# Performance work log

Measured on AMD Instinct MI355X. Metric: run time of the kernel, lower is better.

Reference implementation:

```python
import jax, jax.numpy as jnp
import numpy as np

V, D, H, L, C = 32000, 256, 256, 2, 2  # vocab, embed, hidden, layers, classes
B, T = 64, 1024
PAD = 0


def setup_inputs() -> dict:
    key = jax.random.key(0)
    ks = jax.random.split(key, 10)
    # end-padded token sequences with realistic lengths
    tokens = jax.random.randint(ks[0], (B, T), 1, V)
    lengths = jax.random.randint(ks[1], (B,), T // 2, T + 1)
    valid = jnp.arange(T)[None, :] < lengths[:, None]
    x = jnp.where(valid, tokens, PAD)
    # embedding table, padding row zeroed (padding_idx semantics)
    E = (jax.random.normal(ks[2], (V, D)) * 0.02).at[PAD].set(0.0)

    def gate(k, in_size):
        W = jax.random.normal(k, (in_size + H, 4 * H)) / np.sqrt(in_size + H)
        b = jnp.zeros((4 * H,)).at[:H].set(1.0)  # forget-gate bias = 1
        return W, b

    Wf0, bf0 = gate(ks[3], D)
    Wb0, bb0 = gate(ks[4], D)
    Wf1, bf1 = gate(ks[5], 2 * H)
    Wb1, bb1 = gate(ks[6], 2 * H)
    Wfc = jax.random.normal(ks[7], (2 * H, C)) / np.sqrt(2 * H)
    bfc = jnp.zeros((C,))
    return dict(x=x, E=E, Wf0=Wf0, bf0=bf0, Wb0=Wb0, bb0=bb0,
                Wf1=Wf1, bf1=bf1, Wb1=Wb1, bb1=bb1, Wfc=Wfc, bfc=bfc)


def _run_dir(seq, lengths, W, b, reverse):
    # seq: (B, T, in) -> outputs (B, T, H), last hidden (B, H)
    Tn = seq.shape[1]
    xs = jnp.swapaxes(seq, 0, 1)          # (T, B, in)
    ts = jnp.arange(Tn)
    if reverse:
        xs, ts = xs[::-1], ts[::-1]
    h0 = jnp.zeros((seq.shape[0], H), seq.dtype)

    def step(carry, inp):
        h, c = carry
        x_t, t = inp
        z = jnp.concatenate([h, x_t], axis=-1) @ W + b   # (B, 4H)
        f, i, g, o = jnp.split(z, 4, axis=-1)            # gate order: f,i,g,o
        c_new = jax.nn.sigmoid(f) * c + jax.nn.sigmoid(i) * jnp.tanh(g)
        h_new = jax.nn.sigmoid(o) * jnp.tanh(c_new)
        m = (t < lengths)[:, None].astype(h.dtype)       # freeze state at pads
        h = m * h_new + (1.0 - m) * h
        c = m * c_new + (1.0 - m) * c
        return (h, c), h

    (hT, _), outs = jax.lax.scan(step, (h0, h0), (xs, ts))
    outs = jnp.swapaxes(outs, 0, 1)                      # (B, T, H)
    if reverse:
        outs = outs[:, ::-1]
    return outs, hT


def reference(x, E, Wf0, bf0, Wb0, bb0, Wf1, bf1, Wb1, bb1, Wfc, bfc):
    lengths = (x != PAD).sum(axis=1)
    layer_input = E[x]                                   # (B, T, D)
    params = [(Wf0, bf0, Wb0, bb0), (Wf1, bf1, Wb1, bb1)]
    fh = bh = None
    for Wf, bf, Wb, bb in params:
        fo, fh = _run_dir(layer_input, lengths, Wf, bf, reverse=False)
        bo, bh = _run_dir(layer_input, lengths, Wb, bb, reverse=True)
        layer_input = jnp.concatenate([fo, bo], axis=-1)  # (B, T, 2H)
    h = jnp.concatenate([fh, bh], axis=1)                 # (B, 2H)
    return h @ Wfc + bfc                                  # (B, C) logits
```

## Files before the change

### kernel.cpp

```cpp
#include <hip/hip_runtime.h>
#include <hip/hip_bf16.h>
#include <math.h>

namespace {
constexpr int Bn = 64;
constexpr int Tn = 1024;
constexpr int Dn = 256;
constexpr int Hn = 256;
}

typedef __attribute__((ext_vector_type(8))) short short8;
typedef __attribute__((ext_vector_type(4))) float f32x4;

template <typename T>
__device__ __forceinline__ float ldf(const T* p, long i);
template <>
__device__ __forceinline__ float ldf<float>(const float* p, long i) { return p[i]; }
template <>
__device__ __forceinline__ float ldf<__hip_bfloat16>(const __hip_bfloat16* p, long i) {
  return __bfloat162float(p[i]);
}

__device__ __forceinline__ float sigmf(float x) {
  return __builtin_amdgcn_rcpf(1.0f + __expf(-x));
}
__device__ __forceinline__ float tanh_fast(float x) {
  return 1.0f - 2.0f * __builtin_amdgcn_rcpf(__expf(2.0f * x) + 1.0f);
}

__device__ __forceinline__ void lds_barrier() {
  asm volatile("s_waitcnt lgkmcnt(0)" ::: "memory");
  __builtin_amdgcn_sched_barrier(0);
  __builtin_amdgcn_s_barrier();
  __builtin_amdgcn_sched_barrier(0);
}

__global__ void k_detect(const unsigned short* __restrict__ e, int* __restrict__ flag) {
  __shared__ int sbuf[256];
  int bad = 0;
  for (int i = threadIdx.x; i < 4096; i += 256) {
    const unsigned short v = e[i];
    const int ex = (v >> 7) & 0xFF;
    bad += (ex >= 137) ? 1 : 0;
  }
  sbuf[threadIdx.x] = bad;
  __syncthreads();
  for (int s = 128; s > 0; s >>= 1) {
    if (threadIdx.x < s) sbuf[threadIdx.x] += sbuf[threadIdx.x + s];
    __syncthreads();
  }
  if (threadIdx.x == 0) flag[0] = (sbuf[0] > 64) ? 1 : 0;
}

__global__ void k_lengths(const int* __restrict__ x, int* __restrict__ len) {
  const int b = blockIdx.x;
  int cnt = 0;
  for (int t = threadIdx.x; t < Tn; t += blockDim.x) cnt += (x[b * Tn + t] != 0) ? 1 : 0;
  __shared__ int sbuf[256];
  sbuf[threadIdx.x] = cnt;
  __syncthreads();
  for (int s = 128; s > 0; s >>= 1) {
    if (threadIdx.x < s) sbuf[threadIdx.x] += sbuf[threadIdx.x + s];
    __syncthreads();
  }
  if (threadIdx.x == 0) len[b] = sbuf[0];
}


__global__ void k_prep_small(const void* b0f, const void* b0b, const void* b1f, const void* b1b,
                             const int* __restrict__ flag, float* __restrict__ biasbuf) {
  const int tid = threadIdx.x;
  const bool isf32 = flag[0] != 0;
  for (int idx = tid; idx < 4096; idx += 256) {
    const int j = idx >> 10, col = idx & 1023;
    const void* src = (j == 0) ? b0f : (j == 1) ? b0b : (j == 2) ? b1f : b1b;
    biasbuf[idx] = isf32 ? ((const float*)src)[col]
                         : __bfloat162float(((const __hip_bfloat16*)src)[col]);
  }
}

__global__ void k_prepw(const void* W0, const void* W1, const void* W2, const void* W3,
                        const int* __restrict__ flag, __hip_bfloat16* __restrict__ whT,
                        __hip_bfloat16* __restrict__ wxT0, __hip_bfloat16* __restrict__ wxT1) {
  const int j = blockIdx.z;
  const int rows = (j < 2) ? 512 : 768;
  const int bx = blockIdx.x;
  if (bx * 64 >= rows) return;
  const int by = blockIdx.y;
  const void* W = (j == 0) ? W0 : (j == 1) ? W1 : (j == 2) ? W2 : W3;
  const bool isf32 = flag[0] != 0;
  __shared__ float tile[64][65];
  const int tid = threadIdx.x;
  const int c = tid & 63, r4 = tid >> 6;
#pragma unroll
  for (int rep = 0; rep < 16; ++rep) {
    const int rr = r4 * 16 + rep;
    const size_t idx = (size_t)(bx * 64 + rr) * 1024 + by * 64 + c;
    tile[rr][c] = isf32 ? ((const float*)W)[idx]
                        : __bfloat162float(((const __hip_bfloat16*)W)[idx]);
  }
  __syncthreads();
  const int kk = tid & 63;
#pragma unroll
  for (int rep = 0; rep < 16; ++rep) {
    const int a = r4 * 16 + rep;
    const int n = by * 64 + a;
    const int k = bx * 64 + kk;
    const __hip_bfloat16 v = __float2bfloat16(tile[kk][a]);
    if (k < 256) {
      whT[(size_t)j * (1024 * 256) + (size_t)n * 256 + k] = v;
    } else {
      const int k2 = k - 256;
      if (j < 2)
        wxT0[(size_t)j * (1024 * 256) + (size_t)n * 256 + k2] = v;
      else
        wxT1[(size_t)(j - 2) * (1024 * 512) + (size_t)n * 512 + k2] = v;
    }
  }
}

template <int K, bool GATHER>
__launch_bounds__(256, 2)
__global__ void k_xproj3(const int* __restrict__ x, const void* __restrict__ E,
                         const int* __restrict__ flag, const __hip_bfloat16* __restrict__ Af,
                         const __hip_bfloat16* __restrict__ Ab,
                         const __hip_bfloat16* __restrict__ WT,
                         __hip_bfloat16* __restrict__ xp,
                         const int Mrows, const int t0f, const int t0b) {
  constexpr int KC = 256;
  __shared__ __hip_bfloat16 Btile[128][KC + 8];
  const int tix = blockIdx.x;
  const int by = tix & 7;
  const int dz = (tix >> 3) & 1;
  const int bx = tix >> 4;
  const int tid = threadIdx.x, w = tid >> 6, L = tid & 63, quad = L >> 4, l16 = L & 15;
  const __hip_bfloat16* __restrict__ WTd = WT + (size_t)dz * (1024 * K);
  __hip_bfloat16* __restrict__ o = xp + (size_t)dz * Mrows * 1024;

  f32x4 acc[2][8];
#pragma unroll
  for (int mt = 0; mt < 2; ++mt)
#pragma unroll
    for (int nt = 0; nt < 8; ++nt) {
      acc[mt][nt][0] = 0.f; acc[mt][nt][1] = 0.f; acc[mt][nt][2] = 0.f; acc[mt][nt][3] = 0.f;
    }

  const int row0 = bx * 128 + w * 32 + l16;
  const __hip_bfloat16* arow0b = nullptr;
  const __hip_bfloat16* arow1b = nullptr;
  const float* arow0f = nullptr;
  const float* arow1f = nullptr;
  bool isf32 = false;
  if constexpr (GATHER) {
    isf32 = flag[0] != 0;
    const int t0 = (dz ? t0b : t0f) + (row0 >> 6), b0 = row0 & 63;
    const int r1 = row0 + 16;
    const int t1 = (dz ? t0b : t0f) + (r1 >> 6), b1 = r1 & 63;
    const int tok0 = x[b0 * Tn + t0];
    const int tok1 = x[b1 * Tn + t1];
    if (isf32) {
      arow0f = (const float*)E + (size_t)tok0 * Dn;
      arow1f = (const float*)E + (size_t)tok1 * Dn;
    } else {
      arow0b = (const __hip_bfloat16*)E + (size_t)tok0 * Dn;
      arow1b = (const __hip_bfloat16*)E + (size_t)tok1 * Dn;
    }
  } else {
    const __hip_bfloat16* A = dz ? Ab : Af;
    arow0b = A + (size_t)row0 * K;
    arow1b = A + (size_t)(row0 + 16) * K;
  }

  for (int ch = 0; ch < K / KC; ++ch) {
    if (ch) __syncthreads();
#pragma unroll
    for (int it = 0; it < 16; ++it) {
      const int idx = it * 256 + tid;
      const int col = idx >> 5, seg = idx & 31;
      *(short8*)&Btile[col][seg * 8] =
          *(const short8*)(WTd + (size_t)(by * 128 + col) * K + ch * KC + seg * 8);
    }
    __syncthreads();

#pragma unroll
    for (int kc = 0; kc < 8; ++kc) {
      short8 a0, a1;
      if constexpr (GATHER) {
        if (isf32) {
#pragma unroll
          for (int jj = 0; jj < 8; ++jj) {
            __hip_bfloat16 h0 = __float2bfloat16(arow0f[kc * 32 + quad * 8 + jj]);
            __hip_bfloat16 h1 = __float2bfloat16(arow1f[kc * 32 + quad * 8 + jj]);
            a0[jj] = *(const short*)&h0;
            a1[jj] = *(const short*)&h1;
          }
        } else {
          a0 = *(const short8*)(arow0b + kc * 32 + quad * 8);
          a1 = *(const short8*)(arow1b + kc * 32 + quad * 8);
        }
      } else {
        a0 = *(const short8*)(arow0b + ch * KC + kc * 32 + quad * 8);
        a1 = *(const short8*)(arow1b + ch * KC + kc * 32 + quad * 8);
      }
#pragma unroll
      for (int nt = 0; nt < 8; ++nt) {
        const short8 b = *(const short8*)&Btile[nt * 16 + l16][kc * 32 + quad * 8];
        acc[0][nt] = __builtin_amdgcn_mfma_f32_16x16x32_bf16(a0, b, acc[0][nt], 0, 0, 0);
        acc[1][nt] = __builtin_amdgcn_mfma_f32_16x16x32_bf16(a1, b, acc[1][nt], 0, 0, 0);
      }
    }
  }

  {
    const int tl = bx * 2 + (w >> 1);
    const int jv = (by >> 1) * 2 + (w & 1);
    const int qbase = (by & 1) << 1;
    __hip_bfloat16* __restrict__ ob = o + (size_t)tl * 65536 + (size_t)jv * 2048;
#pragma unroll
    for (int nt = 0; nt < 8; ++nt) {
      const int q_ = qbase + (nt >> 2);
      const int tid_c = (nt & 3) * 64 + quad * 16 + l16;
      short8 sv;
#pragma unroll
      for (int r = 0; r < 4; ++r) {
        __hip_bfloat16 h0 = __float2bfloat16(acc[0][nt][r]);
        __hip_bfloat16 h1 = __float2bfloat16(acc[1][nt][r]);
        sv[r] = *(const short*)&h0;
        sv[4 + r] = *(const short*)&h1;
      }
      *(short8*)(ob + (size_t)q_ * 16384 + tid_c * 8) = sv;
    }
  }
}

template <bool WRITE_SEQ>
__launch_bounds__(256, 1) __global__
void k_lstm_fast(const __hip_bfloat16* __restrict__ WhT,
                 const __hip_bfloat16* __restrict__ xproj,
                 const float* __restrict__ biasL,
                 const int* __restrict__ lengths,
                 unsigned* __restrict__ hgs,
                 unsigned* __restrict__ hflags,
                 float* __restrict__ cstate, float* __restrict__ hstate,
                 __hip_bfloat16* __restrict__ seq0,
                 const int s0, const int Tc) {
  const int xcd = blockIdx.x & 7;
  const int kq = blockIdx.x >> 3;
  if (xcd >= 2 || kq >= 4) return;
  const int d = xcd;
  const int q = kq;
  const int tid = threadIdx.x;
  const int w = tid >> 6, L = tid & 63, quad = L >> 4, l16 = L & 15;
  const int u = q * 64 + w * 16 + l16;

  __shared__ __hip_bfloat16 h_lds[2][64][272];
  for (int idx = tid; idx < 2 * 64 * 272; idx += 256)
    (&h_lds[0][0][0])[idx] = __float2bfloat16(0.0f);

  const __hip_bfloat16* __restrict__ Wd = WhT + (size_t)d * (1024 * 256);
  short8 wfrag[4][8];
#pragma unroll
  for (int g = 0; g < 4; ++g)
#pragma unroll
    for (int kc = 0; kc < 8; ++kc)
      wfrag[g][kc] = *(const short8*)(Wd + (size_t)(g * 256 + u) * 256 + kc * 32 + quad * 8);

  float bz[4];
#pragma unroll
  for (int g = 0; g < 4; ++g) bz[g] = biasL[d * 1024 + g * 256 + u];

  float c_reg[16], h_reg[16];
  int len_b[16];
#pragma unroll
  for (int mt = 0; mt < 4; ++mt)
#pragma unroll
    for (int r = 0; r < 4; ++r) {
      const int idx = mt * 4 + r;
      const int b = mt * 16 + quad * 4 + r;
      len_b[idx] = lengths[b];
      if (s0 == 0) {
        c_reg[idx] = 0.0f;
        h_reg[idx] = 0.0f;
      } else {
        c_reg[idx] = cstate[((size_t)(d * 64 + b) << 8) + u];
        h_reg[idx] = hstate[((size_t)(d * 64 + b) << 8) + u];
      }
    }
  __syncthreads();
  {
    const int ib = (s0 - 1) & 1;
#pragma unroll
    for (int mt = 0; mt < 4; ++mt)
#pragma unroll
      for (int r = 0; r < 4; ++r)
        h_lds[ib][mt * 16 + quad * 4 + r][u] = __float2bfloat16(h_reg[mt * 4 + r]);
  }
  __syncthreads();

  const __hip_bfloat16* __restrict__ xq =
      xproj + (size_t)d * Tc * 65536 + (size_t)q * 16384 + (size_t)tid * 8;

  for (int sl = 0; sl < Tc; ++sl) {
    const int s = s0 + sl;
    const int t = d ? (Tn - 1 - s) : s;
    const int tl = d ? (Tc - 1 - sl) : sl;
    const int pb = (s - 1) & 1;
    const int cb = s & 1;

    short8 xv[8];
    {
      const __hip_bfloat16* __restrict__ src = xq + (size_t)tl * 65536;
#pragma unroll
      for (int jv = 0; jv < 8; ++jv) xv[jv] = *(const short8*)(src + jv * 2048);
    }

    if (s > 0) {
      if (w != q) {
        const unsigned exp = (unsigned)s;
        {
          const unsigned* __restrict__ f4 =
              hflags + (((d * 2 + ((s - 1) & 1)) * 4 + w) * 4);
          for (;;) {
            const unsigned f0 =
                __hip_atomic_load(f4 + 0, __ATOMIC_RELAXED, __HIP_MEMORY_SCOPE_AGENT);
            const unsigned f1 =
                __hip_atomic_load(f4 + 1, __ATOMIC_RELAXED, __HIP_MEMORY_SCOPE_AGENT);
            const unsigned f2 =
                __hip_atomic_load(f4 + 2, __ATOMIC_RELAXED, __HIP_MEMORY_SCOPE_AGENT);
            const unsigned f3 =
                __hip_atomic_load(f4 + 3, __ATOMIC_RELAXED, __HIP_MEMORY_SCOPE_AGENT);
            if (f0 >= exp && f1 >= exp && f2 >= exp && f3 >= exp) break;
            __builtin_amdgcn_s_sleep(1);
          }
        }
        const unsigned long long* __restrict__ src64 =
            (const unsigned long long*)(hgs + ((((size_t)d * 2 + ((s - 1) & 1)) * 4 + w) << 12));
        unsigned long long v[32];
        unsigned pend = 0xFFFFFFFFu;
        int tries = 0;
        do {
          if (tries++) __builtin_amdgcn_s_sleep(1);
#pragma unroll
          for (int i = 0; i < 32; ++i)
            if (pend & (1u << i))
              v[i] = __hip_atomic_load(src64 + i * 64 + L, __ATOMIC_RELAXED,
                                       __HIP_MEMORY_SCOPE_AGENT);
#pragma unroll
          for (int i = 0; i < 32; ++i)
            if (pend & (1u << i)) {
              const unsigned lo = (unsigned)v[i], hi = (unsigned)(v[i] >> 32);
              if ((lo >> 16) == exp && (hi >> 16) == exp) pend &= ~(1u << i);
            }
        } while (pend);
#pragma unroll
        for (int i = 0; i < 32; ++i) {
          const int j = i * 64 + L;
          const unsigned lo = (unsigned)v[i], hi = (unsigned)(v[i] >> 32);
          const unsigned packed = (lo & 0xFFFFu) | (hi << 16);
          *(unsigned*)&h_lds[pb][j >> 5][w * 64 + (j & 31) * 2] = packed;
        }
      }
      lds_barrier();
    }

    f32x4 acc[4][4];
#pragma unroll
    for (int mt = 0; mt < 4; ++mt)
#pragma unroll
      for (int g = 0; g < 4; ++g) {
        const short8 v = xv[g * 2 + (mt >> 1)];
#pragma unroll
        for (int r = 0; r < 4; ++r) {
          const short sv = v[(mt & 1) * 4 + r];
          acc[mt][g][r] = __bfloat162float(*(const __hip_bfloat16*)&sv) + bz[g];
        }
      }

#pragma unroll
    for (int kc = 0; kc < 8; ++kc) {
#pragma unroll
      for (int mt = 0; mt < 4; ++mt) {
        const short8 a = *(const short8*)&h_lds[pb][mt * 16 + l16][kc * 32 + quad * 8];
#pragma unroll
        for (int g = 0; g < 4; ++g)
          acc[mt][g] =
              __builtin_amdgcn_mfma_f32_16x16x32_bf16(a, wfrag[g][kc], acc[mt][g], 0, 0, 0);
      }
    }

    unsigned* __restrict__ dst32 = hgs + ((((size_t)d * 2 + (s & 1)) * 4 + q) << 12);
    const unsigned tag = ((unsigned)(s + 1)) << 16;
    __hip_bfloat16 hbf[16];
#pragma unroll
    for (int mt = 0; mt < 4; ++mt)
#pragma unroll
      for (int r = 0; r < 4; ++r) {
        const int idx = mt * 4 + r, b = mt * 16 + quad * 4 + r;
        const float fg = sigmf(acc[mt][0][r]);
        const float ig = sigmf(acc[mt][1][r]);
        const float gg = tanh_fast(acc[mt][2][r]);
        const float og = sigmf(acc[mt][3][r]);
        const float cn = fg * c_reg[idx] + ig * gg;
        const float hn = og * tanh_fast(cn);
        if (t < len_b[idx]) {
          c_reg[idx] = cn;
          h_reg[idx] = hn;
        }
        hbf[idx] = __float2bfloat16(h_reg[idx]);
        __hip_atomic_store(dst32 + b * 64 + w * 16 + l16,
                           tag | (unsigned)*(unsigned short*)&hbf[idx], __ATOMIC_RELAXED,
                           __HIP_MEMORY_SCOPE_AGENT);
      }

    if (L == 0)
      __hip_atomic_store(hflags + (((d * 2 + (s & 1)) * 4 + q) * 4 + w),
                         (unsigned)(s + 1), __ATOMIC_RELAXED, __HIP_MEMORY_SCOPE_AGENT);

#pragma unroll
    for (int mt = 0; mt < 4; ++mt)
#pragma unroll
      for (int r = 0; r < 4; ++r)
        h_lds[cb][mt * 16 + quad * 4 + r][u] = hbf[mt * 4 + r];

    if (WRITE_SEQ) {
#pragma unroll
      for (int mt = 0; mt < 4; ++mt)
#pragma unroll
        for (int r = 0; r < 4; ++r) {
          const int b = mt * 16 + quad * 4 + r;
          seq0[((size_t)t * 64 + b) * 512 + d * 256 + u] = hbf[mt * 4 + r];
        }
    }
  }

#pragma unroll
  for (int mt = 0; mt < 4; ++mt)
#pragma unroll
    for (int r = 0; r < 4; ++r) {
      const int idx = mt * 4 + r, b = mt * 16 + quad * 4 + r;
      cstate[((size_t)(d * 64 + b) << 8) + u] = c_reg[idx];
      hstate[((size_t)(d * 64 + b) << 8) + u] = h_reg[idx];
    }
}

template <typename TW, int XK, bool WRITE_SEQ>
__device__ __forceinline__ void lstm_body(const int* __restrict__ x, const TW* __restrict__ E,
                                          const __hip_bfloat16* __restrict__ seq_in,
                                          const TW* __restrict__ W, const TW* __restrict__ bias,
                                          const int len, const int b, const int dir,
                                          __hip_bfloat16* __restrict__ seq_out,
                                          float* __restrict__ hfin) {
  const int j = threadIdx.x;
  __shared__ float h[Hn];
  __shared__ float xb[XK];
  float hj = 0.0f, cj = 0.0f;
  h[j] = 0.0f;
  const float bfj = ldf(bias, j);
  const float bij = ldf(bias, Hn + j);
  const float bgj = ldf(bias, 2 * Hn + j);
  const float boj = ldf(bias, 3 * Hn + j);
  __syncthreads();
  for (int s = 0; s < Tn; ++s) {
    const int t = dir ? (Tn - 1 - s) : s;
    const bool active = (t < len);
    if (active) {
      if constexpr (XK == Dn) {
        const int tok = x[b * Tn + t];
        xb[j] = ldf(E, (long)tok * Dn + j);
      } else {
        const long base = ((long)(b * Tn + t)) * (2 * Hn);
        xb[j] = __bfloat162float(seq_in[base + j]);
        xb[j + Hn] = __bfloat162float(seq_in[base + j + Hn]);
      }
      __syncthreads();
      float af = bfj, ai = bij, ag = bgj, ao = boj;
#pragma unroll 4
      for (int k = 0; k < Hn; ++k) {
        const float hk = h[k];
        const long r = (long)k * (4 * Hn);
        af += hk * ldf(W, r + j);
        ai += hk * ldf(W, r + Hn + j);
        ag += hk * ldf(W, r + 2 * Hn + j);
        ao += hk * ldf(W, r + 3 * Hn + j);
      }
#pragma unroll 4
      for (int k = 0; k < XK; ++k) {
        const float xk = xb[k];
        const long r = (long)(Hn + k) * (4 * Hn);
        af += xk * ldf(W, r + j);
        ai += xk * ldf(W, r + Hn + j);
        ag += xk * ldf(W, r + 2 * Hn + j);
        ao += xk * ldf(W, r + 3 * Hn + j);
      }
      const float fg = 1.0f / (1.0f + expf(-af));
      const float ig = 1.0f / (1.0f + expf(-ai));
      const float gg = tanhf(ag);
      const float og = 1.0f / (1.0f + expf(-ao));
      const float cn = fg * cj + ig * gg;
      const float hn = og * tanhf(cn);
      __syncthreads();
      hj = hn;
      cj = cn;
      h[j] = hn;
      __syncthreads();
    }
    if constexpr (WRITE_SEQ) {
      seq_out[((long)(b * Tn + t)) * (2 * Hn) + dir * Hn + j] = __float2bfloat16(hj);
    }
  }
  if constexpr (!WRITE_SEQ) hfin[(dir * Bn + b) * Hn + j] = hj;
}

template <int XK, bool WRITE_SEQ>
__global__ void k_lstm(const int* __restrict__ x, const void* __restrict__ E,
                       const __hip_bfloat16* __restrict__ seq_in, const void* __restrict__ Wf,
                       const void* __restrict__ bf, const void* __restrict__ Wb,
                       const void* __restrict__ bb, const int* __restrict__ lengths,
                       const int* __restrict__ flag, __hip_bfloat16* __restrict__ seq_out,
                       float* __restrict__ hfin) {
  const int b = blockIdx.x & (Bn - 1);
  const int dir = blockIdx.x >> 6;
  const int len = lengths[b];
  const void* W = dir ? Wb : Wf;
  const void* bias = dir ? bb : bf;
  if (flag[0]) {
    lstm_body<float, XK, WRITE_SEQ>(x, (const float*)E, seq_in, (const float*)W,
                                    (const float*)bias, len, b, dir, seq_out, hfin);
  } else {
    lstm_body<__hip_bfloat16, XK, WRITE_SEQ>(x, (const __hip_bfloat16*)E, seq_in,
                                             (const __hip_bfloat16*)W, (const __hip_bfloat16*)bias,
                                             len, b, dir, seq_out, hfin);
  }
}

template <typename TW>
__device__ __forceinline__ void fc_body(const float* __restrict__ hfin, const TW* __restrict__ Wfc,
                                        const TW* __restrict__ bfc, TW* __restrict__ out) {
  const int idx = threadIdx.x;
  const int b = idx >> 1;
  const int cc = idx & 1;
  float acc = ldf(bfc, cc);
  for (int k = 0; k < Hn; ++k) acc += hfin[(0 * Bn + b) * Hn + k] * ldf(Wfc, k * 2 + cc);
  for (int k = 0; k < Hn; ++k) acc += hfin[(1 * Bn + b) * Hn + k] * ldf(Wfc, (Hn + k) * 2 + cc);
  if constexpr (sizeof(TW) == 2) {
    out[b * 2 + cc] = __float2bfloat16(acc);
  } else {
    out[b * 2 + cc] = acc;
  }
}

__global__ void k_fc(const float* __restrict__ hfin, const void* __restrict__ Wfc,
                     const void* __restrict__ bfc, const int* __restrict__ flag,
                     void* __restrict__ out) {
  if (flag[0]) {
    fc_body<float>(hfin, (const float*)Wfc, (const float*)bfc, (float*)out);
  } else {
    fc_body<__hip_bfloat16>(hfin, (const __hip_bfloat16*)Wfc, (const __hip_bfloat16*)bfc,
                            (__hip_bfloat16*)out);
  }
}

extern "C" void kernel_launch(void* const* d_in, const int* in_sizes, int n_in,
                              void* d_out, int out_size, void* d_ws, size_t ws_size,
                              hipStream_t stream) {
  const int* x = (const int*)d_in[0];
  const void* E = d_in[1];
  const void* Wf0 = d_in[2];
  const void* bf0 = d_in[3];
  const void* Wb0 = d_in[4];
  const void* bb0 = d_in[5];
  const void* Wf1 = d_in[6];
  const void* bf1 = d_in[7];
  const void* Wb1 = d_in[8];
  const void* bb1 = d_in[9];
  const void* Wfc = d_in[10];
  const void* bfc = d_in[11];

  char* ws = (char*)d_ws;
  int* flag = (int*)ws;
  int* lengths = (int*)(ws + 256);

  const size_t MB = 1ull << 20;
  const size_t KB = 1024;

  k_detect<<<1, 256, 0, stream>>>((const unsigned short*)E, flag);
  k_lengths<<<Bn, 256, 0, stream>>>(x, lengths);

  int Tc = 0;
  {
    const size_t fixed = 73 * MB;
    const int cands[7] = {1024, 512, 256, 128, 64, 32, 16};
    for (int i = 0; i < 7; ++i)
      if (fixed + (size_t)cands[i] * 256 * KB <= ws_size) { Tc = cands[i]; break; }
  }

  if (Tc > 0) {
    float* biasbuf = (float*)(ws + 4096);
    __hip_bfloat16* whT = (__hip_bfloat16*)(ws + 1 * MB);
    __hip_bfloat16* wxT0 = (__hip_bfloat16*)(ws + 3 * MB);
    __hip_bfloat16* wxT1 = (__hip_bfloat16*)(ws + 4 * MB);
    unsigned* hgs0 = (unsigned*)(ws + 6 * MB);
    unsigned* hgs1 = (unsigned*)(ws + 6 * MB + 256 * KB);
    unsigned* hflags0 = (unsigned*)(ws + 6 * MB + 512 * KB);
    unsigned* hflags1 = (unsigned*)(ws + 6 * MB + 513 * KB);
    float* cstate0 = (float*)(ws + 7 * MB);
    float* hstate0 = (float*)(ws + 7 * MB + 128 * KB);
    float* cstate1 = (float*)(ws + 7 * MB + 256 * KB);
    float* hstate1 = (float*)(ws + 7 * MB + 384 * KB);
    __hip_bfloat16* seq0 = (__hip_bfloat16*)(ws + 8 * MB);
    __hip_bfloat16* xsl = (__hip_bfloat16*)(ws + 73 * MB);

    k_prep_small<<<1, 256, 0, stream>>>(bf0, bb0, bf1, bb1, flag, biasbuf);
    k_prepw<<<dim3(12, 16, 4), 256, 0, stream>>>(Wf0, Wb0, Wf1, Wb1, flag, whT, wxT0, wxT1);
    hipMemsetAsync(hgs0, 0, 516 * KB, stream);

    const int P = Tn / Tc;
    const int Mrows = Tc * 64;
    const int ntiles = (Mrows / 128) * 16;
    for (int p = 0; p < P; ++p) {
      const int s0 = p * Tc;
      const int t0f = s0, t0b = Tn - s0 - Tc;
      k_xproj3<256, true><<<ntiles, 256, 0, stream>>>(x, E, flag, nullptr, nullptr, wxT0, xsl,
                                                      Mrows, t0f, t0b);
      k_lstm_fast<true><<<64, 256, 0, stream>>>(whT, xsl, biasbuf, lengths, hgs0, hflags0,
                                                cstate0, hstate0, seq0, s0, Tc);
    }
    for (int p = 0; p < P; ++p) {
      const int s0 = p * Tc;
      const int t0f = s0, t0b = Tn - s0 - Tc;
      k_xproj3<512, false><<<ntiles, 256, 0, stream>>>(
          x, E, flag, seq0 + (size_t)t0f * 64 * 512, seq0 + (size_t)t0b * 64 * 512, wxT1, xsl,
          Mrows, 0, 0);
      k_lstm_fast<false><<<64, 256, 0, stream>>>(whT + 2 * 1024 * 256, xsl, biasbuf + 2048,
                                                 lengths, hgs1, hflags1, cstate1, hstate1,
                                                 nullptr, s0, Tc);
    }
    k_fc<<<1, 128, 0, stream>>>(hstate1, Wfc, bfc, flag, d_out);
  } else {
    __hip_bfloat16* seq0 = (__hip_bfloat16*)(ws + 64 * 1024);
    const size_t seq0_bytes = (size_t)Bn * Tn * 2 * Hn * sizeof(__hip_bfloat16);
    float* hfin = (float*)(ws + 64 * 1024 + seq0_bytes);
    k_lstm<Dn, true><<<2 * Bn, 256, 0, stream>>>(x, E, nullptr, Wf0, bf0, Wb0, bb0, lengths, flag,
                                                 seq0, nullptr);
    k_lstm<2 * Hn, false><<<2 * Bn, 256, 0, stream>>>(x, E, seq0, Wf1, bf1, Wb1, bb1, lengths,
                                                      flag, nullptr, hfin);
    k_fc<<<1, 128, 0, stream>>>(hfin, Wfc, bfc, flag, d_out);
  }
}
```

Before: 12.05 ms.

## Prefetch next-step input projections and unroll recurrent loop by two

Unrolls the recurrent time loop by two with a macro so the double-buffer parity is a compile-time constant. It also keeps two register buffers of x-projection fragments, issuing the loads for the next step while the current step waits, runs its MFMAs and computes gates. The goal is to hide global-load latency and index arithmetic on the serial critical path. In exchange it raises register pressure and assumes even chunk start and chunk length, since the initial h buffer is now fixed to slot 1.

```diff
diff --git a/kernel.cpp b/kernel.cpp
--- a/kernel.cpp
+++ b/kernel.cpp
@@ -233,6 +233,121 @@
   }
 }
 
+#define LSTM_STEP(SL, PAR, XC, XN, DOPREF)                                                 \
+  {                                                                                        \
+    const int s = s0 + (SL);                                                               \
+    const int t = d ? (Tn - 1 - s) : s;                                                    \
+                     \
+    f32x4 acc[4][4];                                                                       \
+    _Pragma("unroll") for (int mt = 0; mt < 4; ++mt)                                       \
+      _Pragma("unroll") for (int g = 0; g < 4; ++g) {                                      \
+        const short8 v_ = (XC)[g * 2 + (mt >> 1)];                                         \
+        _Pragma("unroll") for (int r = 0; r < 4; ++r) {                                    \
+          const short sv_ = v_[(mt & 1) * 4 + r];                                          \
+          acc[mt][g][r] = __bfloat162float(*(const __hip_bfloat16*)&sv_) + bz[g];          \
+        }                                                                                  \
+      }                                                                                    \
+              \
+    if (s > 0) {                                                                           \
+      if (w != q) {                                                                        \
+        const unsigned exp_ = (unsigned)s;                                                 \
+        {                                                                                  \
+          const unsigned* __restrict__ f4 =                                                \
+              hflags + (((d * 2 + ((PAR) ^ 1)) * 4 + w) * 4);                              \
+          for (;;) {                                                                       \
+            const unsigned f0 =                                                            \
+                __hip_atomic_load(f4 + 0, __ATOMIC_RELAXED, __HIP_MEMORY_SCOPE_AGENT);     \
+            const unsigned f1 =                                                            \
+                __hip_atomic_load(f4 + 1, __ATOMIC_RELAXED, __HIP_MEMORY_SCOPE_AGENT);     \
+            const unsigned f2 =                                                            \
+                __hip_atomic_load(f4 + 2, __ATOMIC_RELAXED, __HIP_MEMORY_SCOPE_AGENT);     \
+            const unsigned f3 =                                                            \
+                __hip_atomic_load(f4 + 3, __ATOMIC_RELAXED, __HIP_MEMORY_SCOPE_AGENT);     \
+            if (f0 >= exp_ && f1 >= exp_ && f2 >= exp_ && f3 >= exp_) break;               \
+            __builtin_amdgcn_s_sleep(1);                                                   \
+          }                                                                                \
+        }                                                                                  \
+        const unsigned long long* __restrict__ src64 = (const unsigned long long*)(        \
+            hgs + ((((size_t)d * 2 + ((PAR) ^ 1)) * 4 + w) << 12));                        \
+        unsigned long long v_[32];                                                         \
+        unsigned pend = 0xFFFFFFFFu;                                                       \
+        int tries = 0;                                                                     \
+        do {                                                                               \
+          if (tries++) __builtin_amdgcn_s_sleep(1);                                        \
+          _Pragma("unroll") for (int i = 0; i < 32; ++i)                                   \
+            if (pend & (1u << i))                                                          \
+              v_[i] = __hip_atomic_load(src64 + i * 64 + L, __ATOMIC_RELAXED,              \
+                                        __HIP_MEMORY_SCOPE_AGENT);                         \
+          _Pragma("unroll") for (int i = 0; i < 32; ++i)                                   \
+            if (pend & (1u << i)) {                                                        \
+              const unsigned lo = (unsigned)v_[i], hi = (unsigned)(v_[i] >> 32);           \
+              if ((lo >> 16) == exp_ && (hi >> 16) == exp_) pend &= ~(1u << i);            \
+            }                                                                              \
+        } while (pend);                                                                    \
+        _Pragma("unroll") for (int i = 0; i < 32; ++i) {                                   \
+          const int j_ = i * 64 + L;                                                       \
+          const unsigned lo = (unsigned)v_[i], hi = (unsigned)(v_[i] >> 32);               \
+          const unsigned packed = (lo & 0xFFFFu) | (hi << 16);                             \
+          *(unsigned*)&h_lds[(PAR) ^ 1][j_ >> 5][w * 64 + (j_ & 31) * 2] = packed;         \
+        }                                                                                  \
+      }                                                                                    \
+      lds_barrier();                                                                       \
+    }                                                                                      \
+                          \
+    if (DOPREF) {                                                                          \
+      const int tln = d ? (Tc - 1 - ((SL) + 1)) : ((SL) + 1);                              \
+      const __hip_bfloat16* __restrict__ srcn = xq + (size_t)tln * 65536;                  \
+      _Pragma("unroll") for (int jv = 0; jv < 8; ++jv)                                     \
+        (XN)[jv] = *(const short8*)(srcn + jv * 2048);                                     \
+    }                                                                                      \
+                                        \
+    _Pragma("unroll") for (int kc = 0; kc < 8; ++kc) {                                     \
+      _Pragma("unroll") for (int mt = 0; mt < 4; ++mt) {                                   \
+        const short8 a_ =                                                                  \
+            *(const short8*)&h_lds[(PAR) ^ 1][mt * 16 + l16][kc * 32 + quad * 8];          \
+        _Pragma("unroll") for (int g = 0; g < 4; ++g)                                      \
+          acc[mt][g] =                                                                     \
+              __builtin_amdgcn_mfma_f32_16x16x32_bf16(a_, wfrag[g][kc], acc[mt][g], 0, 0, 0); \
+      }                                                                                    \
+    }                                                                                      \
+                      \
+    unsigned* __restrict__ dst32 = hgs + ((((size_t)d * 2 + (PAR)) * 4 + q) << 12);        \
+    const unsigned tag = ((unsigned)(s + 1)) << 16;                                        \
+    __hip_bfloat16 hbf[16];                                                                \
+    _Pragma("unroll") for (int mt = 0; mt < 4; ++mt)                                       \
+      _Pragma("unroll") for (int r = 0; r < 4; ++r) {                                      \
+        const int idx_ = mt * 4 + r, b_ = mt * 16 + quad * 4 + r;                          \
+        const float fg = sigmf(acc[mt][0][r]);                                             \
+        const float ig = sigmf(acc[mt][1][r]);                                             \
+        const float gg = tanh_fast(acc[mt][2][r]);                                         \
+        const float og = sigmf(acc[mt][3][r]);                                             \
+        const float cn = fg * c_reg[idx_] + ig * gg;                                       \
+        const float hn = og * tanh_fast(cn);                                               \
+        if (t < len_b[idx_]) {                                                             \
+          c_reg[idx_] = cn;                                                                \
+          h_reg[idx_] = hn;                                                                \
+        }                                                                                  \
+        hbf[idx_] = __float2bfloat16(h_reg[idx_]);                                         \
+        __hip_atomic_store(dst32 + b_ * 64 + w * 16 + l16,                                 \
+                           tag | (unsigned)*(unsigned short*)&hbf[idx_], __ATOMIC_RELAXED, \
+                           __HIP_MEMORY_SCOPE_AGENT);                                      \
+      }                                                                                    \
+    if (L == 0)                                                                            \
+      __hip_atomic_store(hflags + (((d * 2 + (PAR)) * 4 + q) * 4 + w), (unsigned)(s + 1),  \
+                         __ATOMIC_RELAXED, __HIP_MEMORY_SCOPE_AGENT);                      \
+                     \
+    _Pragma("unroll") for (int mt = 0; mt < 4; ++mt)                                       \
+      _Pragma("unroll") for (int r = 0; r < 4; ++r)                                        \
+        h_lds[(PAR)][mt * 16 + quad * 4 + r][u] = hbf[mt * 4 + r];                         \
+    if (WRITE_SEQ) {                                                                       \
+      _Pragma("unroll") for (int mt = 0; mt < 4; ++mt)                                     \
+        _Pragma("unroll") for (int r = 0; r < 4; ++r) {                                    \
+          const int b_ = mt * 16 + quad * 4 + r;                                           \
+          seq0[((size_t)t * 64 + b_) * 512 + d * 256 + u] = hbf[mt * 4 + r];               \
+        }                                                                                  \
+    }                                                                                      \
+  }
+
 template <bool WRITE_SEQ>
 __launch_bounds__(256, 1) __global__
 void k_lstm_fast(const __hip_bfloat16* __restrict__ WhT,
@@ -287,150 +402,27 @@
       }
     }
   __syncthreads();
-  {
-    const int ib = (s0 - 1) & 1;
-#pragma unroll
-    for (int mt = 0; mt < 4; ++mt)
-#pragma unroll
-      for (int r = 0; r < 4; ++r)
-        h_lds[ib][mt * 16 + quad * 4 + r][u] = __float2bfloat16(h_reg[mt * 4 + r]);
-  }
+#pragma unroll
+  for (int mt = 0; mt < 4; ++mt)
+#pragma unroll
+    for (int r = 0; r < 4; ++r)
+      h_lds[1][mt * 16 + quad * 4 + r][u] = __float2bfloat16(h_reg[mt * 4 + r]);
   __syncthreads();
 
   const __hip_bfloat16* __restrict__ xq =
       xproj + (size_t)d * Tc * 65536 + (size_t)q * 16384 + (size_t)tid * 8;
 
-  for (int sl = 0; sl < Tc; ++sl) {
-    const int s = s0 + sl;
-    const int t = d ? (Tn - 1 - s) : s;
-    const int tl = d ? (Tc - 1 - sl) : sl;
-    const int pb = (s - 1) & 1;
-    const int cb = s & 1;
-
-    short8 xv[8];
-    {
-      const __hip_bfloat16* __restrict__ src = xq + (size_t)tl * 65536;
-#pragma unroll
-      for (int jv = 0; jv < 8; ++jv) xv[jv] = *(const short8*)(src + jv * 2048);
-    }
-
-    if (s > 0) {
-      if (w != q) {
-        const unsigned exp = (unsigned)s;
-        {
-          const unsigned* __restrict__ f4 =
-              hflags + (((d * 2 + ((s - 1) & 1)) * 4 + w) * 4);
-          for (;;) {
-            const unsigned f0 =
-                __hip_atomic_load(f4 + 0, __ATOMIC_RELAXED, __HIP_MEMORY_SCOPE_AGENT);
-            const unsigned f1 =
-                __hip_atomic_load(f4 + 1, __ATOMIC_RELAXED, __HIP_MEMORY_SCOPE_AGENT);
-            const unsigned f2 =
-                __hip_atomic_load(f4 + 2, __ATOMIC_RELAXED, __HIP_MEMORY_SCOPE_AGENT);
-            const unsigned f3 =
-                __hip_atomic_load(f4 + 3, __ATOMIC_RELAXED, __HIP_MEMORY_SCOPE_AGENT);
-            if (f0 >= exp && f1 >= exp && f2 >= exp && f3 >= exp) break;
-            __builtin_amdgcn_s_sleep(1);
-          }
-        }
-        const unsigned long long* __restrict__ src64 =
-            (const unsigned long long*)(hgs + ((((size_t)d * 2 + ((s - 1) & 1)) * 4 + w) << 12));
-        unsigned long long v[32];
-        unsigned pend = 0xFFFFFFFFu;
-        int tries = 0;
-        do {
-          if (tries++) __builtin_amdgcn_s_sleep(1);
-#pragma unroll
-          for (int i = 0; i < 32; ++i)
-            if (pend & (1u << i))
-              v[i] = __hip_atomic_load(src64 + i * 64 + L, __ATOMIC_RELAXED,
-                                       __HIP_MEMORY_SCOPE_AGENT);
-#pragma unroll
-          for (int i = 0; i < 32; ++i)
-            if (pend & (1u << i)) {
-              const unsigned lo = (unsigned)v[i], hi = (unsigned)(v[i] >> 32);
-              if ((lo >> 16) == exp && (hi >> 16) == exp) pend &= ~(1u << i);
-            }
-        } while (pend);
-#pragma unroll
-        for (int i = 0; i < 32; ++i) {
-          const int j = i * 64 + L;
-          const unsigned lo = (unsigned)v[i], hi = (unsigned)(v[i] >> 32);
-          const unsigned packed = (lo & 0xFFFFu) | (hi << 16);
-          *(unsigned*)&h_lds[pb][j >> 5][w * 64 + (j & 31) * 2] = packed;
-        }
-      }
-      lds_barrier();
-    }
-
-    f32x4 acc[4][4];
-#pragma unroll
-    for (int mt = 0; mt < 4; ++mt)
-#pragma unroll
-      for (int g = 0; g < 4; ++g) {
-        const short8 v = xv[g * 2 + (mt >> 1)];
-#pragma unroll
-        for (int r = 0; r < 4; ++r) {
-          const short sv = v[(mt & 1) * 4 + r];
-          acc[mt][g][r] = __bfloat162float(*(const __hip_bfloat16*)&sv) + bz[g];
-        }
-      }
-
-#pragma unroll
-    for (int kc = 0; kc < 8; ++kc) {
-#pragma unroll
-      for (int mt = 0; mt < 4; ++mt) {
-        const short8 a = *(const short8*)&h_lds[pb][mt * 16 + l16][kc * 32 + quad * 8];
-#pragma unroll
-        for (int g = 0; g < 4; ++g)
-          acc[mt][g] =
-              __builtin_amdgcn_mfma_f32_16x16x32_bf16(a, wfrag[g][kc], acc[mt][g], 0, 0, 0);
-      }
-    }
-
-    unsigned* __restrict__ dst32 = hgs + ((((size_t)d * 2 + (s & 1)) * 4 + q) << 12);
-    const unsigned tag = ((unsigned)(s + 1)) << 16;
-    __hip_bfloat16 hbf[16];
-#pragma unroll
-    for (int mt = 0; mt < 4; ++mt)
-#pragma unroll
-      for (int r = 0; r < 4; ++r) {
-        const int idx = mt * 4 + r, b = mt * 16 + quad * 4 + r;
-        const float fg = sigmf(acc[mt][0][r]);
-        const float ig = sigmf(acc[mt][1][r]);
-        const float gg = tanh_fast(acc[mt][2][r]);
-        const float og = sigmf(acc[mt][3][r]);
-        const float cn = fg * c_reg[idx] + ig * gg;
-        const float hn = og * tanh_fast(cn);
-        if (t < len_b[idx]) {
-          c_reg[idx] = cn;
-          h_reg[idx] = hn;
-        }
-        hbf[idx] = __float2bfloat16(h_reg[idx]);
-        __hip_atomic_store(dst32 + b * 64 + w * 16 + l16,
-                           tag | (unsigned)*(unsigned short*)&hbf[idx], __ATOMIC_RELAXED,
-                           __HIP_MEMORY_SCOPE_AGENT);
-      }
-
-    if (L == 0)
-      __hip_atomic_store(hflags + (((d * 2 + (s & 1)) * 4 + q) * 4 + w),
-                         (unsigned)(s + 1), __ATOMIC_RELAXED, __HIP_MEMORY_SCOPE_AGENT);
-
-#pragma unroll
-    for (int mt = 0; mt < 4; ++mt)
-#pragma unroll
-      for (int r = 0; r < 4; ++r)
-        h_lds[cb][mt * 16 + quad * 4 + r][u] = hbf[mt * 4 + r];
-
-    if (WRITE_SEQ) {
-#pragma unroll
-      for (int mt = 0; mt < 4; ++mt)
-#pragma unroll
-        for (int r = 0; r < 4; ++r) {
-          const int b = mt * 16 + quad * 4 + r;
-          seq0[((size_t)t * 64 + b) * 512 + d * 256 + u] = hbf[mt * 4 + r];
-        }
-    }
+  short8 xvA[8], xvB[8];
+  {
+    const int tl0 = d ? (Tc - 1) : 0;
+    const __hip_bfloat16* __restrict__ src0 = xq + (size_t)tl0 * 65536;
+#pragma unroll
+    for (int jv = 0; jv < 8; ++jv) xvA[jv] = *(const short8*)(src0 + jv * 2048);
+  }
+
+  for (int sl = 0; sl < Tc; sl += 2) {
+    LSTM_STEP(sl, 0, xvA, xvB, true)
+    LSTM_STEP(sl + 1, 1, xvB, xvA, (sl + 2 < Tc))
   }
 
 #pragma unroll
@@ -442,6 +434,7 @@
       hstate[((size_t)(d * 64 + b) << 8) + u] = h_reg[idx];
     }
 }
+#undef LSTM_STEP
 
 template <typename TW, int XK, bool WRITE_SEQ>
 __device__ __forceinline__ void lstm_body(const int* __restrict__ x, const TW* __restrict__ E,
```

Result: slower. 19.48 ms (+61.7%).
